# Performance work log

Hardware: AMD Instinct MI355X
Metric: run time of the kernel (lower is better)

Reference implementation:

```python
import jax, jax.numpy as jnp
import numpy as np

NEG_SLOPE = 0.2


def gat_layer(x, src, dst, W, attn_l, attn_r, bias):
    # x: [N, in_dim]; W: [in_dim, H*D]; attn_l/attn_r/bias: [H, D] / [H, D] / [H, D]
    N = x.shape[0]
    H, D = attn_l.shape
    feat = (x @ W).reshape(N, H, D)                      # [N, H, D]
    el = jnp.sum(feat * attn_l, axis=-1)                 # [N, H]
    er = jnp.sum(feat * attn_r, axis=-1)                 # [N, H]
    e = jax.nn.leaky_relu(el[src] + er[dst], NEG_SLOPE)  # [E, H]
    # edge softmax over incoming edges of each dst node (numerically stable)
    emax = jax.ops.segment_max(e, dst, num_segments=N)   # [N, H]
    ex = jnp.exp(e - emax[dst])                          # [E, H]
    denom = jax.ops.segment_sum(ex, dst, num_segments=N) # [N, H]
    alpha = ex / denom[dst]                              # [E, H]
    msg = alpha[:, :, None] * feat[src]                  # [E, H, D]
    rst = jax.ops.segment_sum(msg, dst, num_segments=N)  # [N, H, D]
    return rst + bias


def setup_inputs() -> dict:
    key = jax.random.key(0)
    ks = jax.random.split(key, 16)
    N, E = 50000, 800000
    IN, H, D, C = 128, 8, 16, 10
    HD = H * D  # 128
    s = lambda fan: 1.0 / np.sqrt(fan)
    return {
        "x": jax.random.normal(ks[0], (N, IN), jnp.float32),
        "src": jax.random.randint(ks[1], (E,), 0, N, jnp.int32),
        "dst": jax.random.randint(ks[2], (E,), 0, N, jnp.int32),
        "W1": jax.random.normal(ks[3], (IN, HD), jnp.float32) * s(IN),
        "al1": jax.random.normal(ks[4], (H, D), jnp.float32) * s(D),
        "ar1": jax.random.normal(ks[5], (H, D), jnp.float32) * s(D),
        "b1": jnp.zeros((H, D), jnp.float32),
        "W2": jax.random.normal(ks[6], (HD, HD), jnp.float32) * s(HD),
        "al2": jax.random.normal(ks[7], (H, D), jnp.float32) * s(D),
        "ar2": jax.random.normal(ks[8], (H, D), jnp.float32) * s(D),
        "b2": jnp.zeros((H, D), jnp.float32),
        "Wc": jax.random.normal(ks[9], (HD, C), jnp.float32) * s(HD),
        "bc": jnp.zeros((C,), jnp.float32),
    }


def reference(x, src, dst, W1, al1, ar1, b1, W2, al2, ar2, b2, Wc, bc):
    N = x.shape[0]
    h = gat_layer(x, src, dst, W1, al1, ar1, b1)       # [N, H, D]
    h = jax.nn.relu(h).reshape(N, -1)                  # [N, H*D]
    h = gat_layer(h, src, dst, W2, al2, ar2, b2)       # [N, H, D]
    hg = jnp.mean(h, axis=0).reshape(1, -1)            # mean_nodes, single graph -> [1, H*D]
    return hg @ Wc + bc                                # [1, num_classes]
```

## Files before the change

### kernel.cpp

```cpp
#include <hip/hip_runtime.h>
#include <hip/hip_bf16.h>

#define LEAKY 0.2f
#define BINB 8
#define TILE 2048
#define CAP 8192

static inline int ceil_div(int a, int b) { return (a + b - 1) / b; }

typedef __bf16 bf16x8 __attribute__((ext_vector_type(8)));
typedef float f32x4 __attribute__((ext_vector_type(4)));

__device__ __forceinline__ ushort f2bf(float f) {
    unsigned int x = __float_as_uint(f);
    unsigned int r = (x + 0x7fffu + ((x >> 16) & 1u)) >> 16;
    return (ushort)r;
}


__global__ __launch_bounds__(256) void bin_count(const int* __restrict__ dst,
                                                 int* __restrict__ bin_cnt, int E, int NB) {
    __shared__ int h[256];
    int t = threadIdx.x;
    h[t] = 0;
    __syncthreads();
    int base = blockIdx.x * TILE;
#pragma unroll
    for (int j = 0; j < TILE / 256; ++j) {
        int i = base + j * 256 + t;
        if (i < E) atomicAdd(&h[dst[i] >> BINB], 1);
    }
    __syncthreads();
    if (t < NB && h[t]) atomicAdd(&bin_cnt[t], h[t]);
}

__global__ __launch_bounds__(256) void bin_scan(const int* __restrict__ bin_cnt,
                                                int* __restrict__ binStart,
                                                int* __restrict__ bin_cursor,
                                                int* __restrict__ rowstart,
                                                int NB, int N, int E) {
    __shared__ int s[256];
    int t = threadIdx.x;
    int v = (t < NB) ? bin_cnt[t] : 0;
    s[t] = v;
    __syncthreads();
    for (int off = 1; off < 256; off <<= 1) {
        int x = (t >= off) ? s[t - off] : 0;
        __syncthreads();
        s[t] += x;
        __syncthreads();
    }
    int excl = s[t] - v;
    if (t < NB) {
        binStart[t] = excl;
        bin_cursor[t] = excl;
        if (t == NB - 1) binStart[NB] = excl + v;
    }
    if (t == 0) rowstart[N] = E;
}

__global__ __launch_bounds__(256) void bin_scatter(const int* __restrict__ src,
                                                   const int* __restrict__ dst,
                                                   int* __restrict__ bin_cursor,
                                                   unsigned int* __restrict__ coarse, int E) {
    __shared__ int hist[256], scn[256], gbase[256], lcur[256];
    __shared__ unsigned int outp[TILE];
    __shared__ int gidx[TILE];
    int t = threadIdx.x;
    hist[t] = 0;
    __syncthreads();
    int base = blockIdx.x * TILE;
    int dloc[TILE / 256];
#pragma unroll
    for (int j = 0; j < TILE / 256; ++j) {
        int i = base + j * 256 + t;
        int d = (i < E) ? dst[i] : -1;
        dloc[j] = d;
        if (d >= 0) atomicAdd(&hist[d >> BINB], 1);
    }
    __syncthreads();
    int hv = hist[t];
    scn[t] = hv;
    __syncthreads();
    for (int off = 1; off < 256; off <<= 1) {
        int x = (t >= off) ? scn[t - off] : 0;
        __syncthreads();
        scn[t] += x;
        __syncthreads();
    }
    int excl = scn[t] - hv;
    if (hv > 0) gbase[t] = atomicAdd(&bin_cursor[t], hv);
    lcur[t] = excl;
    scn[t] = excl;
    __syncthreads();
#pragma unroll
    for (int j = 0; j < TILE / 256; ++j) {
        int i = base + j * 256 + t;
        int d = dloc[j];
        if (d >= 0) {
            int b = d >> BINB;
            int pos = atomicAdd(&lcur[b], 1);
            outp[pos] = (unsigned int)src[i] | ((unsigned int)(d & ((1 << BINB) - 1)) << 16);
            gidx[pos] = gbase[b] + (pos - scn[b]);
        }
    }
    __syncthreads();
    int cnt = min(TILE, E - base);
    for (int j = t; j < cnt; j += 256) coarse[gidx[j]] = outp[j];
}

__global__ __launch_bounds__(256) void fine_csr(const unsigned int* __restrict__ coarse,
                                                const int* __restrict__ binStart,
                                                int* __restrict__ rowstart,
                                                ushort* __restrict__ bucket, int N) {
    __shared__ int hist[256], scn[256], cur[256];
    __shared__ ushort sb[CAP];
    int b = blockIdx.x, t = threadIdx.x;
    int e0 = binStart[b], e1 = binStart[b + 1];
    int cnt = e1 - e0;
    hist[t] = 0;
    __syncthreads();
    for (int j = e0 + t; j < e1; j += 256) atomicAdd(&hist[coarse[j] >> 16], 1);
    __syncthreads();
    int hv = hist[t];
    scn[t] = hv;
    __syncthreads();
    for (int off = 1; off < 256; off <<= 1) {
        int x = (t >= off) ? scn[t - off] : 0;
        __syncthreads();
        scn[t] += x;
        __syncthreads();
    }
    int excl = scn[t] - hv;
    int n = (b << BINB) + t;
    if (n < N) rowstart[n] = e0 + excl;
    cur[t] = excl;
    __syncthreads();
    bool fit = (cnt <= CAP);
    for (int j = e0 + t; j < e1; j += 256) {
        unsigned int p = coarse[j];
        int dl = p >> 16;
        int pos = atomicAdd(&cur[dl], 1);
        ushort sv = (ushort)(p & 0xffffu);
        if (fit) sb[pos] = sv;
        else bucket[e0 + pos] = sv;
    }
    __syncthreads();
    if (fit)
        for (int j = t; j < cnt; j += 256) bucket[e0 + j] = sb[j];
}

__global__ __launch_bounds__(256) void convert_w(const float* __restrict__ W1,
                                                 const float* __restrict__ W2,
                                                 ushort* __restrict__ Wt1,
                                                 ushort* __restrict__ Wt2) {
    int idx = blockIdx.x * 256 + threadIdx.x;
    const float* W = (idx < 16384) ? W1 : W2;
    ushort* O = (idx < 16384) ? Wt1 : Wt2;
    int i = idx & 16383;
    int k = i >> 7, n = i & 127;
    O[n * 128 + k] = f2bf(W[i]);
}

#define LDK 136
template <bool BF16IN>
__global__ __launch_bounds__(256) void gemm_attn_mfma(const void* __restrict__ in_,
                                                      const ushort* __restrict__ Wt,
                                                      const float* __restrict__ al,
                                                      const float* __restrict__ ar,
                                                      ushort* __restrict__ feat,
                                                      float* __restrict__ el,
                                                      float* __restrict__ er, int N) {
    __shared__ ushort sA[64 * LDK];
    int tid = threadIdx.x;
    int rowbase = blockIdx.x * 64;

    if (BF16IN) {
        const ushort* in = (const ushort*)in_;
#pragma unroll
        for (int i = 0; i < 4; ++i) {
            int idx8 = i * 256 + tid;
            int flat = idx8 * 8;
            int row = flat >> 7, col = flat & 127;
            int grow = rowbase + row;
            uint4 v = make_uint4(0, 0, 0, 0);
            if (grow < N) v = *reinterpret_cast<const uint4*>(in + (size_t)grow * 128 + col);
            *reinterpret_cast<uint4*>(&sA[row * LDK + col]) = v;
        }
    } else {
        const float* in = (const float*)in_;
#pragma unroll
        for (int i = 0; i < 8; ++i) {
            int idx4 = i * 256 + tid;
            int flat = idx4 * 4;
            int row = flat >> 7, col = flat & 127;
            int grow = rowbase + row;
            float4 v = make_float4(0.f, 0.f, 0.f, 0.f);
            if (grow < N) v = *reinterpret_cast<const float4*>(in + (size_t)grow * 128 + col);
            uint2 w;
            w.x = (unsigned int)f2bf(v.x) | ((unsigned int)f2bf(v.y) << 16);
            w.y = (unsigned int)f2bf(v.z) | ((unsigned int)f2bf(v.w) << 16);
            *reinterpret_cast<uint2*>(&sA[row * LDK + col]) = w;
        }
    }
    __syncthreads();

    int wid = tid >> 6;
    int lane = tid & 63;
    int wm = wid >> 1;
    int wn = wid & 1;
    int l15 = lane & 15;
    int lhi = lane >> 4;

    f32x4 acc[2][4] = {};
    const ushort* wb = Wt + (size_t)(wn * 64 + l15) * 128 + lhi * 8;
    const ushort* a0p = &sA[(wm * 32 + l15) * LDK + lhi * 8];
    const ushort* a1p = &sA[(wm * 32 + 16 + l15) * LDK + lhi * 8];

#pragma unroll
    for (int ks = 0; ks < 4; ++ks) {
        bf16x8 a0 = *reinterpret_cast<const bf16x8*>(a0p + ks * 32);
        bf16x8 a1 = *reinterpret_cast<const bf16x8*>(a1p + ks * 32);
#pragma unroll
        for (int ni = 0; ni < 4; ++ni) {
            bf16x8 b = *reinterpret_cast<const bf16x8*>(wb + ni * 16 * 128 + ks * 32);
            acc[0][ni] = __builtin_amdgcn_mfma_f32_16x16x32_bf16(a0, b, acc[0][ni], 0, 0, 0);
            acc[1][ni] = __builtin_amdgcn_mfma_f32_16x16x32_bf16(a1, b, acc[1][ni], 0, 0, 0);
        }
    }

#pragma unroll
    for (int ni = 0; ni < 4; ++ni) {
        int head = wn * 4 + ni;
        float alv = al[head * 16 + l15];
        float arv = ar[head * 16 + l15];
#pragma unroll
        for (int mi = 0; mi < 2; ++mi) {
#pragma unroll
            for (int reg = 0; reg < 4; ++reg) {
                int row = rowbase + wm * 32 + mi * 16 + lhi * 4 + reg;
                float v = acc[mi][ni][reg];
                float pl = v * alv;
                float pr = v * arv;
#pragma unroll
                for (int off = 8; off; off >>= 1) {
                    pl += __shfl_xor(pl, off);
                    pr += __shfl_xor(pr, off);
                }
                if (row < N) {
                    feat[(size_t)row * 128 + head * 16 + l15] = f2bf(v);
                    if (l15 == 0) {
                        el[row * 8 + head] = pl;
                        er[row * 8 + head] = pr;
                    }
                }
            }
        }
    }
}

__global__ __launch_bounds__(256) void aggregate(const ushort* __restrict__ feat,
                                                 const float* __restrict__ el,
                                                 const float* __restrict__ er,
                                                 const int* __restrict__ rowstart,
                                                 const ushort* __restrict__ bucket,
                                                 const float* __restrict__ bias,
                                                 ushort* __restrict__ out,
                                                 int N, int do_relu) {
    __shared__ float pl[4][64];
    int w = threadIdx.x >> 6;
    int wid = (blockIdx.x * 256 + threadIdx.x) >> 6;
    int lane = threadIdx.x & 63;
    if (wid >= N) return;
    int l7 = lane & 7;
    int e8 = lane >> 3;
    int h = e8;
    float erv = er[wid * 8 + l7];
    int beg = rowstart[wid];
    int end = rowstart[wid + 1];

    const unsigned int* fp = reinterpret_cast<const unsigned int*>(feat) + lane;

    float lsum = 0.0f, ax = 0.0f, ay = 0.0f;

    for (int base = beg; base < end; base += 8) {
        int j1 = base + e8;
        bool v1 = j1 < end;
        int s1 = (int)bucket[v1 ? j1 : beg];
        float e = el[s1 * 8 + l7] + erv;
        e = (e > 0.0f) ? e : LEAKY * e;
        float pv = v1 ? __expf(e) : 0.0f;
        pl[w][lane] = pv;

        int cnt = min(8, end - base);
        if (cnt == 8) {
#pragma unroll
            for (int q = 0; q < 8; ++q) {
                int s = (int)bucket[base + q];
                float pq = pl[w][q * 8 + h];
                unsigned int u = fp[s * 64];
                lsum += pq;
                ax = fmaf(pq, __uint_as_float(u << 16), ax);
                ay = fmaf(pq, __uint_as_float(u & 0xffff0000u), ay);
            }
        } else {
            for (int q = 0; q < cnt; ++q) {
                int s = (int)bucket[base + q];
                float pq = pl[w][q * 8 + h];
                unsigned int u = fp[s * 64];
                lsum += pq;
                ax = fmaf(pq, __uint_as_float(u << 16), ax);
                ay = fmaf(pq, __uint_as_float(u & 0xffff0000u), ay);
            }
        }
    }

    float inv = (end > beg) ? 1.0f / lsum : 0.0f;

    int c = lane * 2;
    float2 bv = *reinterpret_cast<const float2*>(bias + c);
    float ox = fmaf(ax, inv, bv.x);
    float oy = fmaf(ay, inv, bv.y);
    if (do_relu) {
        ox = fmaxf(ox, 0.0f);
        oy = fmaxf(oy, 0.0f);
    }
    unsigned int pk = (unsigned int)f2bf(ox) | ((unsigned int)f2bf(oy) << 16);
    reinterpret_cast<unsigned int*>(out)[(size_t)wid * 64 + lane] = pk;
}

__global__ __launch_bounds__(256) void mean_reduce(const ushort* __restrict__ h,
                                                   float* __restrict__ meanbuf, int N) {
    int c = threadIdx.x & 127;
    int rbase = blockIdx.x * 2 + (threadIdx.x >> 7);
    float s = 0.0f;
    for (int r = rbase; r < N; r += gridDim.x * 2)
        s += __uint_as_float((unsigned int)h[(size_t)r * 128 + c] << 16);
    atomicAdd(&meanbuf[c], s);
}

__global__ __launch_bounds__(64) void classifier(const float* __restrict__ meanbuf,
                                                 const float* __restrict__ Wc,
                                                 const float* __restrict__ bc,
                                                 float* __restrict__ outp, float invN) {
    int j = threadIdx.x;
    if (j < 10) {
        float s = 0.0f;
        for (int k = 0; k < 128; ++k) s += meanbuf[k] * invN * Wc[k * 10 + j];
        outp[j] = s + bc[j];
    }
}


extern "C" void kernel_launch(void* const* d_in, const int* in_sizes, int n_in,
                              void* d_out, int out_size, void* d_ws, size_t ws_size,
                              hipStream_t stream) {
    const float* x   = (const float*)d_in[0];
    const int*   src = (const int*)d_in[1];
    const int*   dst = (const int*)d_in[2];
    const float* W1  = (const float*)d_in[3];
    const float* al1 = (const float*)d_in[4];
    const float* ar1 = (const float*)d_in[5];
    const float* b1  = (const float*)d_in[6];
    const float* W2  = (const float*)d_in[7];
    const float* al2 = (const float*)d_in[8];
    const float* ar2 = (const float*)d_in[9];
    const float* b2  = (const float*)d_in[10];
    const float* Wc  = (const float*)d_in[11];
    const float* bc  = (const float*)d_in[12];

    int N = in_sizes[0] / 128;
    int E = in_sizes[1];
    int NB = (N + (1 << BINB) - 1) >> BINB;

    size_t off = 0;
    auto alloc = [&](size_t bytes) -> void* {
        void* p = (char*)d_ws + off;
        off += (bytes + 255) & ~size_t(255);
        return p;
    };
    int*   bin_cnt    = (int*)alloc(sizeof(int) * NB);
    int*   binStart   = (int*)alloc(sizeof(int) * (NB + 1));
    int*   bin_cursor = (int*)alloc(sizeof(int) * NB);
    int*   rowstart   = (int*)alloc(sizeof(int) * (N + 1));
    unsigned int* coarse = (unsigned int*)alloc(sizeof(unsigned int) * E);
    ushort* bucket  = (ushort*)alloc(sizeof(ushort) * E);
    ushort* feat    = (ushort*)alloc(sizeof(ushort) * (size_t)N * 128);
    float* el       = (float*)alloc(sizeof(float) * N * 8);
    float* er       = (float*)alloc(sizeof(float) * N * 8);
    ushort* h1      = (ushort*)alloc(sizeof(ushort) * (size_t)N * 128);
    ushort* h2      = (ushort*)alloc(sizeof(ushort) * (size_t)N * 128);
    float* meanbuf  = (float*)alloc(sizeof(float) * 128);
    ushort* Wt1     = (ushort*)alloc(sizeof(ushort) * 128 * 128);
    ushort* Wt2     = (ushort*)alloc(sizeof(ushort) * 128 * 128);

    hipMemsetAsync(bin_cnt, 0, sizeof(int) * NB, stream);
    hipMemsetAsync(meanbuf, 0, sizeof(float) * 128, stream);

    int GB = ceil_div(E, TILE);

    bin_count<<<GB, 256, 0, stream>>>(dst, bin_cnt, E, NB);
    bin_scan<<<1, 256, 0, stream>>>(bin_cnt, binStart, bin_cursor, rowstart, NB, N, E);
    bin_scatter<<<GB, 256, 0, stream>>>(src, dst, bin_cursor, coarse, E);
    fine_csr<<<NB, 256, 0, stream>>>(coarse, binStart, rowstart, bucket, N);
    convert_w<<<128, 256, 0, stream>>>(W1, W2, Wt1, Wt2);

    gemm_attn_mfma<false><<<ceil_div(N, 64), 256, 0, stream>>>(x, Wt1, al1, ar1, feat, el, er, N);
    aggregate<<<ceil_div(N * 64, 256), 256, 0, stream>>>(feat, el, er, rowstart, bucket, b1, h1, N, 1);
    gemm_attn_mfma<true><<<ceil_div(N, 64), 256, 0, stream>>>(h1, Wt2, al2, ar2, feat, el, er, N);
    aggregate<<<ceil_div(N * 64, 256), 256, 0, stream>>>(feat, el, er, rowstart, bucket, b2, h2, N, 0);
    mean_reduce<<<256, 256, 0, stream>>>(h2, meanbuf, N);
    classifier<<<1, 64, 0, stream>>>(meanbuf, Wc, bc, (float*)d_out, 1.0f / (float)N);
}
```

Baseline: 241.9 us.

## Store features head-major and aggregate per head with 16-edge parallel waves

Switches feat, el, er and the hidden activations to a head-major [H][N][16] layout, so the per-head slices are contiguous. The aggregation kernel becomes one block per (node group, head): each wave walks 32 nodes in turn, spreads 16 edges across lane groups and reduces with shuffles. Each head's working set (feat slice of about 1.6 MB plus el) is now small enough to stay cache-resident during the random gathers. The cost is 32-byte gathers per edge instead of full 256-byte rows, a serial loop over nodes per wave, and more shuffle reductions. The GEMM input loads and mean_reduce are updated to the new layout, and mean_reduce now reads strided rows.

```diff
diff --git a/kernel.cpp b/kernel.cpp
--- a/kernel.cpp
+++ b/kernel.cpp
@@ -5,6 +5,8 @@
 #define BINB 8
 #define TILE 2048
 #define CAP 8192
+#define NPB 128
+#define NPW 32
 
 static inline int ceil_div(int a, int b) { return (a + b - 1) / b; }
 
@@ -16,6 +18,8 @@
     unsigned int r = (x + 0x7fffu + ((x >> 16) & 1u)) >> 16;
     return (ushort)r;
 }
+__device__ __forceinline__ float bflo(unsigned int u) { return __uint_as_float(u << 16); }
+__device__ __forceinline__ float bfhi(unsigned int u) { return __uint_as_float(u & 0xffff0000u); }
 
 
 __global__ __launch_bounds__(256) void bin_count(const int* __restrict__ dst,
@@ -183,8 +187,10 @@
             int flat = idx8 * 8;
             int row = flat >> 7, col = flat & 127;
             int grow = rowbase + row;
+            int hh = col >> 4, d = col & 15;
             uint4 v = make_uint4(0, 0, 0, 0);
-            if (grow < N) v = *reinterpret_cast<const uint4*>(in + (size_t)grow * 128 + col);
+            if (grow < N)
+                v = *reinterpret_cast<const uint4*>(in + ((size_t)hh * N + grow) * 16 + d);
             *reinterpret_cast<uint4*>(&sA[row * LDK + col]) = v;
         }
     } else {
@@ -248,10 +254,10 @@
                     pr += __shfl_xor(pr, off);
                 }
                 if (row < N) {
-                    feat[(size_t)row * 128 + head * 16 + l15] = f2bf(v);
+                    feat[((size_t)head * N + row) * 16 + l15] = f2bf(v);
                     if (l15 == 0) {
-                        el[row * 8 + head] = pl;
-                        er[row * 8 + head] = pr;
+                        el[(size_t)head * N + row] = pl;
+                        er[(size_t)head * N + row] = pr;
                     }
                 }
             }
@@ -259,83 +265,85 @@
     }
 }
 
-__global__ __launch_bounds__(256) void aggregate(const ushort* __restrict__ feat,
-                                                 const float* __restrict__ el,
-                                                 const float* __restrict__ er,
+__global__ __launch_bounds__(256) void aggregate(const ushort* __restrict__ feat_s,
+                                                 const float* __restrict__ el_t,
+                                                 const float* __restrict__ er_t,
                                                  const int* __restrict__ rowstart,
                                                  const ushort* __restrict__ bucket,
                                                  const float* __restrict__ bias,
-                                                 ushort* __restrict__ out,
+                                                 ushort* __restrict__ out_s,
                                                  int N, int do_relu) {
-    __shared__ float pl[4][64];
+    int h = blockIdx.x & 7;
+    int g = blockIdx.x >> 3;
     int w = threadIdx.x >> 6;
-    int wid = (blockIdx.x * 256 + threadIdx.x) >> 6;
     int lane = threadIdx.x & 63;
-    if (wid >= N) return;
-    int l7 = lane & 7;
-    int e8 = lane >> 3;
-    int h = e8;
-    float erv = er[wid * 8 + l7];
-    int beg = rowstart[wid];
-    int end = rowstart[wid + 1];
-
-    const unsigned int* fp = reinterpret_cast<const unsigned int*>(feat) + lane;
-
-    float lsum = 0.0f, ax = 0.0f, ay = 0.0f;
-
-    for (int base = beg; base < end; base += 8) {
-        int j1 = base + e8;
-        bool v1 = j1 < end;
-        int s1 = (int)bucket[v1 ? j1 : beg];
-        float e = el[s1 * 8 + l7] + erv;
-        e = (e > 0.0f) ? e : LEAKY * e;
-        float pv = v1 ? __expf(e) : 0.0f;
-        pl[w][lane] = pv;
-
-        int cnt = min(8, end - base);
-        if (cnt == 8) {
-#pragma unroll
-            for (int q = 0; q < 8; ++q) {
-                int s = (int)bucket[base + q];
-                float pq = pl[w][q * 8 + h];
-                unsigned int u = fp[s * 64];
-                lsum += pq;
-                ax = fmaf(pq, __uint_as_float(u << 16), ax);
-                ay = fmaf(pq, __uint_as_float(u & 0xffff0000u), ay);
-            }
-        } else {
-            for (int q = 0; q < cnt; ++q) {
-                int s = (int)bucket[base + q];
-                float pq = pl[w][q * 8 + h];
-                unsigned int u = fp[s * 64];
-                lsum += pq;
-                ax = fmaf(pq, __uint_as_float(u << 16), ax);
-                ay = fmaf(pq, __uint_as_float(u & 0xffff0000u), ay);
-            }
-        }
-    }
-
-    float inv = (end > beg) ? 1.0f / lsum : 0.0f;
-
-    int c = lane * 2;
-    float2 bv = *reinterpret_cast<const float2*>(bias + c);
-    float ox = fmaf(ax, inv, bv.x);
-    float oy = fmaf(ay, inv, bv.y);
-    if (do_relu) {
-        ox = fmaxf(ox, 0.0f);
-        oy = fmaxf(oy, 0.0f);
-    }
-    unsigned int pk = (unsigned int)f2bf(ox) | ((unsigned int)f2bf(oy) << 16);
-    reinterpret_cast<unsigned int*>(out)[(size_t)wid * 64 + lane] = pk;
+    int eg = lane >> 2;
+    int dl = lane & 3;
+
+    const float* elh = el_t + (size_t)h * N;
+    const float* erh = er_t + (size_t)h * N;
+    const uint2* fs = reinterpret_cast<const uint2*>(feat_s) + (size_t)h * N * 4 + dl;
+    uint2* os = reinterpret_cast<uint2*>(out_s) + (size_t)h * N * 4;
+    float4 bv = *reinterpret_cast<const float4*>(bias + h * 16 + dl * 4);
+
+    int n0 = g * NPB + w * NPW;
+    int n1 = min(n0 + NPW, N);
+
+    for (int n = n0; n < n1; ++n) {
+        int beg = rowstart[n];
+        int end = rowstart[n + 1];
+        float erv = erh[n];
+        float ax = 0.f, ay = 0.f, az = 0.f, aw = 0.f, lsum = 0.f;
+
+        for (int base = beg; base < end; base += 16) {
+            int j = base + eg;
+            bool vld = j < end;
+            int s = (int)bucket[vld ? j : beg];
+            float e = elh[s] + erv;
+            e = (e > 0.0f) ? e : LEAKY * e;
+            float p = vld ? __expf(e) : 0.0f;
+            lsum += p;
+            uint2 u = fs[(size_t)s * 4];
+            ax = fmaf(p, bflo(u.x), ax);
+            ay = fmaf(p, bfhi(u.x), ay);
+            az = fmaf(p, bflo(u.y), az);
+            aw = fmaf(p, bfhi(u.y), aw);
+        }
+
+#pragma unroll
+        for (int m = 4; m <= 32; m <<= 1) {
+            ax += __shfl_xor(ax, m);
+            ay += __shfl_xor(ay, m);
+            az += __shfl_xor(az, m);
+            aw += __shfl_xor(aw, m);
+            lsum += __shfl_xor(lsum, m);
+        }
+        float inv = (end > beg) ? 1.0f / lsum : 0.0f;
+        float o0 = fmaf(ax, inv, bv.x);
+        float o1 = fmaf(ay, inv, bv.y);
+        float o2 = fmaf(az, inv, bv.z);
+        float o3 = fmaf(aw, inv, bv.w);
+        if (do_relu) {
+            o0 = fmaxf(o0, 0.f); o1 = fmaxf(o1, 0.f);
+            o2 = fmaxf(o2, 0.f); o3 = fmaxf(o3, 0.f);
+        }
+        if (lane < 4) {
+            uint2 pk;
+            pk.x = (unsigned int)f2bf(o0) | ((unsigned int)f2bf(o1) << 16);
+            pk.y = (unsigned int)f2bf(o2) | ((unsigned int)f2bf(o3) << 16);
+            os[(size_t)n * 4 + lane] = pk;
+        }
+    }
 }
 
 __global__ __launch_bounds__(256) void mean_reduce(const ushort* __restrict__ h,
                                                    float* __restrict__ meanbuf, int N) {
     int c = threadIdx.x & 127;
+    int hh = c >> 4, d = c & 15;
     int rbase = blockIdx.x * 2 + (threadIdx.x >> 7);
     float s = 0.0f;
     for (int r = rbase; r < N; r += gridDim.x * 2)
-        s += __uint_as_float((unsigned int)h[(size_t)r * 128 + c] << 16);
+        s += __uint_as_float((unsigned int)h[((size_t)hh * N + r) * 16 + d] << 16);
     atomicAdd(&meanbuf[c], s);
 }
 
@@ -398,6 +406,7 @@
     hipMemsetAsync(meanbuf, 0, sizeof(float) * 128, stream);
 
     int GB = ceil_div(E, TILE);
+    int AGG = ceil_div(N, NPB) * 8;
 
     bin_count<<<GB, 256, 0, stream>>>(dst, bin_cnt, E, NB);
     bin_scan<<<1, 256, 0, stream>>>(bin_cnt, binStart, bin_cursor, rowstart, NB, N, E);
@@ -406,9 +415,9 @@
     convert_w<<<128, 256, 0, stream>>>(W1, W2, Wt1, Wt2);
 
     gemm_attn_mfma<false><<<ceil_div(N, 64), 256, 0, stream>>>(x, Wt1, al1, ar1, feat, el, er, N);
-    aggregate<<<ceil_div(N * 64, 256), 256, 0, stream>>>(feat, el, er, rowstart, bucket, b1, h1, N, 1);
+    aggregate<<<AGG, 256, 0, stream>>>(feat, el, er, rowstart, bucket, b1, h1, N, 1);
     gemm_attn_mfma<true><<<ceil_div(N, 64), 256, 0, stream>>>(h1, Wt2, al2, ar2, feat, el, er, N);
-    aggregate<<<ceil_div(N * 64, 256), 256, 0, stream>>>(feat, el, er, rowstart, bucket, b2, h2, N, 0);
+    aggregate<<<AGG, 256, 0, stream>>>(feat, el, er, rowstart, bucket, b2, h2, N, 0);
     mean_reduce<<<256, 256, 0, stream>>>(h2, meanbuf, N);
     classifier<<<1, 64, 0, stream>>>(meanbuf, Wc, bc, (float*)d_out, 1.0f / (float)N);
 }
```

After: 371.9 us, median of 2. 1.54x slower.

## Precompute edge attention weights in separate kernel and batch gathers in aggregate

Applied to the files above, without the earlier changes.

Fine CSR construction now also records a 16-bit destination per sorted edge. A new edge_weights kernel computes exp(leaky_relu(el[src]+er[dst])) for every edge and head into a float buffer before each aggregation. The aggregate kernel then loads the sources for 64 edges at once, broadcasts them with shuffles, and issues 8 independent weight and feature gathers per step for more memory-level parallelism. The cost is an extra kernel launch and an extra E*8 float buffer (about 25.6 MB) written and read back per layer. Weights stay unnormalised and unmax-shifted, as before.

```diff
diff --git a/kernel.cpp b/kernel.cpp
--- a/kernel.cpp
+++ b/kernel.cpp
@@ -16,6 +16,8 @@
     unsigned int r = (x + 0x7fffu + ((x >> 16) & 1u)) >> 16;
     return (ushort)r;
 }
+__device__ __forceinline__ float bflo(unsigned int u) { return __uint_as_float(u << 16); }
+__device__ __forceinline__ float bfhi(unsigned int u) { return __uint_as_float(u & 0xffff0000u); }
 
 
 __global__ __launch_bounds__(256) void bin_count(const int* __restrict__ dst,
@@ -112,9 +114,11 @@
 __global__ __launch_bounds__(256) void fine_csr(const unsigned int* __restrict__ coarse,
                                                 const int* __restrict__ binStart,
                                                 int* __restrict__ rowstart,
-                                                ushort* __restrict__ bucket, int N) {
+                                                ushort* __restrict__ bucket,
+                                                ushort* __restrict__ dst16, int N) {
     __shared__ int hist[256], scn[256], cur[256];
     __shared__ ushort sb[CAP];
+    __shared__ ushort db[CAP];
     int b = blockIdx.x, t = threadIdx.x;
     int e0 = binStart[b], e1 = binStart[b + 1];
     int cnt = e1 - e0;
@@ -142,12 +146,22 @@
         int dl = p >> 16;
         int pos = atomicAdd(&cur[dl], 1);
         ushort sv = (ushort)(p & 0xffffu);
-        if (fit) sb[pos] = sv;
-        else bucket[e0 + pos] = sv;
-    }
-    __syncthreads();
-    if (fit)
-        for (int j = t; j < cnt; j += 256) bucket[e0 + j] = sb[j];
+        ushort dv = (ushort)((b << BINB) | dl);
+        if (fit) {
+            sb[pos] = sv;
+            db[pos] = dv;
+        } else {
+            bucket[e0 + pos] = sv;
+            dst16[e0 + pos] = dv;
+        }
+    }
+    __syncthreads();
+    if (fit) {
+        for (int j = t; j < cnt; j += 256) {
+            bucket[e0 + j] = sb[j];
+            dst16[e0 + j] = db[j];
+        }
+    }
 }
 
 __global__ __launch_bounds__(256) void convert_w(const float* __restrict__ W1,
@@ -259,74 +273,85 @@
     }
 }
 
+__global__ __launch_bounds__(256) void edge_weights(const ushort* __restrict__ bucket,
+                                                    const ushort* __restrict__ dst16,
+                                                    const float* __restrict__ el,
+                                                    const float* __restrict__ er,
+                                                    float* __restrict__ w, int E) {
+    int tid0 = blockIdx.x * 256 + threadIdx.x;
+    int h = tid0 & 7;
+    int stride = (gridDim.x * 256) >> 3;
+    for (int j = tid0 >> 3; j < E; j += stride) {
+        int s = (int)bucket[j];
+        int d = (int)dst16[j];
+        float x = el[s * 8 + h] + er[d * 8 + h];
+        x = (x > 0.f) ? x : LEAKY * x;
+        w[(size_t)j * 8 + h] = __expf(x);
+    }
+}
+
 __global__ __launch_bounds__(256) void aggregate(const ushort* __restrict__ feat,
-                                                 const float* __restrict__ el,
-                                                 const float* __restrict__ er,
+                                                 const float* __restrict__ w,
                                                  const int* __restrict__ rowstart,
                                                  const ushort* __restrict__ bucket,
                                                  const float* __restrict__ bias,
                                                  ushort* __restrict__ out,
                                                  int N, int do_relu) {
-    __shared__ float pl[4][64];
-    int w = threadIdx.x >> 6;
     int wid = (blockIdx.x * 256 + threadIdx.x) >> 6;
     int lane = threadIdx.x & 63;
     if (wid >= N) return;
-    int l7 = lane & 7;
-    int e8 = lane >> 3;
-    int h = e8;
-    float erv = er[wid * 8 + l7];
+    int h = lane >> 3;
     int beg = rowstart[wid];
     int end = rowstart[wid + 1];
 
     const unsigned int* fp = reinterpret_cast<const unsigned int*>(feat) + lane;
-
-    float lsum = 0.0f, ax = 0.0f, ay = 0.0f;
-
-    for (int base = beg; base < end; base += 8) {
-        int j1 = base + e8;
-        bool v1 = j1 < end;
-        int s1 = (int)bucket[v1 ? j1 : beg];
-        float e = el[s1 * 8 + l7] + erv;
-        e = (e > 0.0f) ? e : LEAKY * e;
-        float pv = v1 ? __expf(e) : 0.0f;
-        pl[w][lane] = pv;
-
-        int cnt = min(8, end - base);
-        if (cnt == 8) {
+    const float* wh = w + h;
+
+    float lsum = 0.f, ax = 0.f, ay = 0.f;
+
+    for (int base = beg; base < end; base += 64) {
+        int cnt = min(end - base, 64);
+        int myedge = base + lane;
+        int sv = (myedge < end) ? (int)bucket[myedge] : 0;
+        int k = 0;
+        for (; k + 8 <= cnt; k += 8) {
+            int ss[8];
+            float ww[8];
+            unsigned int uu[8];
+#pragma unroll
+            for (int q = 0; q < 8; ++q) ss[q] = __shfl(sv, k + q);
+#pragma unroll
+            for (int q = 0; q < 8; ++q) ww[q] = wh[(size_t)(base + k + q) * 8];
+#pragma unroll
+            for (int q = 0; q < 8; ++q) uu[q] = fp[(size_t)ss[q] * 64];
 #pragma unroll
             for (int q = 0; q < 8; ++q) {
-                int s = (int)bucket[base + q];
-                float pq = pl[w][q * 8 + h];
-                unsigned int u = fp[s * 64];
-                lsum += pq;
-                ax = fmaf(pq, __uint_as_float(u << 16), ax);
-                ay = fmaf(pq, __uint_as_float(u & 0xffff0000u), ay);
+                lsum += ww[q];
+                ax = fmaf(ww[q], bflo(uu[q]), ax);
+                ay = fmaf(ww[q], bfhi(uu[q]), ay);
             }
-        } else {
-            for (int q = 0; q < cnt; ++q) {
-                int s = (int)bucket[base + q];
-                float pq = pl[w][q * 8 + h];
-                unsigned int u = fp[s * 64];
-                lsum += pq;
-                ax = fmaf(pq, __uint_as_float(u << 16), ax);
-                ay = fmaf(pq, __uint_as_float(u & 0xffff0000u), ay);
-            }
+        }
+        for (; k < cnt; ++k) {
+            int s = __shfl(sv, k);
+            float wv = wh[(size_t)(base + k) * 8];
+            unsigned int u = fp[(size_t)s * 64];
+            lsum += wv;
+            ax = fmaf(wv, bflo(u), ax);
+            ay = fmaf(wv, bfhi(u), ay);
         }
     }
 
     float inv = (end > beg) ? 1.0f / lsum : 0.0f;
-
     int c = lane * 2;
     float2 bv = *reinterpret_cast<const float2*>(bias + c);
     float ox = fmaf(ax, inv, bv.x);
     float oy = fmaf(ay, inv, bv.y);
     if (do_relu) {
-        ox = fmaxf(ox, 0.0f);
-        oy = fmaxf(oy, 0.0f);
-    }
-    unsigned int pk = (unsigned int)f2bf(ox) | ((unsigned int)f2bf(oy) << 16);
-    reinterpret_cast<unsigned int*>(out)[(size_t)wid * 64 + lane] = pk;
+        ox = fmaxf(ox, 0.f);
+        oy = fmaxf(oy, 0.f);
+    }
+    reinterpret_cast<unsigned int*>(out)[(size_t)wid * 64 + lane] =
+        (unsigned int)f2bf(ox) | ((unsigned int)f2bf(oy) << 16);
 }
 
 __global__ __launch_bounds__(256) void mean_reduce(const ushort* __restrict__ h,
@@ -385,6 +410,8 @@
     int*   rowstart   = (int*)alloc(sizeof(int) * (N + 1));
     unsigned int* coarse = (unsigned int*)alloc(sizeof(unsigned int) * E);
     ushort* bucket  = (ushort*)alloc(sizeof(ushort) * E);
+    ushort* dst16   = (ushort*)alloc(sizeof(ushort) * E);
+    float* wbuf     = (float*)alloc(sizeof(float) * (size_t)E * 8);
     ushort* feat    = (ushort*)alloc(sizeof(ushort) * (size_t)N * 128);
     float* el       = (float*)alloc(sizeof(float) * N * 8);
     float* er       = (float*)alloc(sizeof(float) * N * 8);
@@ -402,13 +429,15 @@
     bin_count<<<GB, 256, 0, stream>>>(dst, bin_cnt, E, NB);
     bin_scan<<<1, 256, 0, stream>>>(bin_cnt, binStart, bin_cursor, rowstart, NB, N, E);
     bin_scatter<<<GB, 256, 0, stream>>>(src, dst, bin_cursor, coarse, E);
-    fine_csr<<<NB, 256, 0, stream>>>(coarse, binStart, rowstart, bucket, N);
+    fine_csr<<<NB, 256, 0, stream>>>(coarse, binStart, rowstart, bucket, dst16, N);
     convert_w<<<128, 256, 0, stream>>>(W1, W2, Wt1, Wt2);
 
     gemm_attn_mfma<false><<<ceil_div(N, 64), 256, 0, stream>>>(x, Wt1, al1, ar1, feat, el, er, N);
-    aggregate<<<ceil_div(N * 64, 256), 256, 0, stream>>>(feat, el, er, rowstart, bucket, b1, h1, N, 1);
+    edge_weights<<<2048, 256, 0, stream>>>(bucket, dst16, el, er, wbuf, E);
+    aggregate<<<ceil_div(N * 64, 256), 256, 0, stream>>>(feat, wbuf, rowstart, bucket, b1, h1, N, 1);
     gemm_attn_mfma<true><<<ceil_div(N, 64), 256, 0, stream>>>(h1, Wt2, al2, ar2, feat, el, er, N);
-    aggregate<<<ceil_div(N * 64, 256), 256, 0, stream>>>(feat, el, er, rowstart, bucket, b2, h2, N, 0);
+    edge_weights<<<2048, 256, 0, stream>>>(bucket, dst16, el, er, wbuf, E);
+    aggregate<<<ceil_div(N * 64, 256), 256, 0, stream>>>(feat, wbuf, rowstart, bucket, b2, h2, N, 0);
     mean_reduce<<<256, 256, 0, stream>>>(h2, meanbuf, N);
     classifier<<<1, 64, 0, stream>>>(meanbuf, Wc, bc, (float*)d_out, 1.0f / (float)N);
 }
```

Result: no change. 240.4 us (-0.6%).
